# Performance work log

Measured on AMD Instinct MI355X. Metric: run time of the kernel, lower is better.

The kernel has to match this reference:

```python
import jax, jax.numpy as jnp
import numpy as np

B, D, K = 32768, 32, 32


def setup_inputs() -> dict:
    key = jax.random.key(0)
    k_x, k_w1, k_w2, k_w3, k_b = jax.random.split(key, 5)
    return {
        "X": jax.random.normal(k_x, (B, D), dtype=jnp.float32),
        "W1": jax.random.normal(k_w1, (D, K), dtype=jnp.float32) * 0.1,
        "W2": jax.random.normal(k_w2, (D, D, K), dtype=jnp.float32) * 0.05,
        "W3": jax.random.normal(k_w3, (D, D, D, K), dtype=jnp.float32) * 0.02,
        "bias": jax.random.normal(k_b, (1, K), dtype=jnp.float32) * 0.1,
    }


def reference(X, W1, W2, W3, bias):
    # order-1 term: addmm(bias, X, W1)  -> [B, K]
    out = bias + X @ W1
    # per-sample outer product X_b X_b^T, [B, D, D]. The torch code builds the
    # full cross-batch mode_dot tensor and keeps only the diagonal
    # (einsum('iik->ik')); mathematically that equals this direct contraction.
    outer = jnp.einsum("bi,bj->bij", X, X)
    out = out + jnp.einsum("bij,ijk->bk", outer, W2)
    # order-3 trilinear term: staged to avoid [B,D,D,D] intermediates.
    t3 = jnp.einsum("bij,ijkl->bkl", outer, W3)  # [B, D, K]
    out = out + jnp.einsum("bkl,bk->bl", t3, X)  # [B, K]
    return out
```

## Files before the change

### kernel.cpp

```cpp
#include <hip/hip_runtime.h>
#include <hip/hip_fp16.h>


typedef __attribute__((ext_vector_type(8))) _Float16 f16x8;
typedef __attribute__((ext_vector_type(16))) float f32x16;

#define NPAIR 561
#define NB 4
#define PAIR_BYTES 2560
#define BATCH_BYTES (NB * PAIR_BYTES)
#define NBATCH 36

union H2V { __half2 h2[4]; f16x8 v; };

__global__ void ntl_prep(const float* __restrict__ W1, const float* __restrict__ W2,
                         const float* __restrict__ W3, __half* __restrict__ Gimg) {
    int tid = blockIdx.x * 256 + threadIdx.x;
    if (tid >= NPAIR * 40 * 32) return;
    int col = tid & 31;
    int k   = (tid >> 5) % 40;
    int m   = tid / (40 * 32);
    int i = 0, rem = m;
    while (rem >= 33 - i) { rem -= 33 - i; ++i; }
    int j = i + rem;
    float v = 0.f;
    if (k < 32) {
        if (j < 32) {
            v = W3[((i * 32 + j) * 32 + k) * 32 + col];
            if (i != j) v += W3[((j * 32 + i) * 32 + k) * 32 + col];
        } else if (i < 32) {
            v = W2[(i * 32 + k) * 32 + col];
        } else {
            v = W1[k * 32 + col];
        }
    }
    Gimg[m * 1280 + col * 40 + k] = __float2half(v);
}

__global__ __launch_bounds__(512, 2) void ntl_main(const float* __restrict__ X,
                                                   const float* __restrict__ bias,
                                                   const __half* __restrict__ Gimg,
                                                   float* __restrict__ out) {
    __shared__ __half xbuf[128 * 34];
    __shared__ __align__(16) unsigned char gbuf[4][2][BATCH_BYTES];

    const int tid = (int)threadIdx.x;
    const int w   = tid >> 6;
    const int l   = tid & 63;
    const int g   = w >> 1;
    const int gw  = w & 1;
    const int h   = l >> 5;
    const int lr  = l & 31;
    const long rowbase = (long)blockIdx.x * 128;

    for (int idx = tid; idx < 128 * 32; idx += 512) {
        int r = idx >> 5, c = idx & 31;
        xbuf[r * 34 + c] = __float2half(X[(rowbase + r) * 32 + c]);
    }
    if (tid < 128) xbuf[tid * 34 + 32] = __float2half(1.0f);

    __half2 xk0[8], xk1[8];
#define LOADX(XK, TROW)                                                          \
    {                                                                            \
        const float* xp = X + (rowbase + gw * 64 + (TROW) + lr) * 32;            \
        float4 f0 = *(const float4*)(xp + 8 * h);                                \
        float4 f1 = *(const float4*)(xp + 8 * h + 4);                            \
        float4 f2 = *(const float4*)(xp + 16 + 8 * h);                           \
        float4 f3 = *(const float4*)(xp + 16 + 8 * h + 4);                       \
        XK[0] = __halves2half2(__float2half(f0.x), __float2half(f0.y));          \
        XK[1] = __halves2half2(__float2half(f0.z), __float2half(f0.w));          \
        XK[2] = __halves2half2(__float2half(f1.x), __float2half(f1.y));          \
        XK[3] = __halves2half2(__float2half(f1.z), __float2half(f1.w));          \
        XK[4] = __halves2half2(__float2half(f2.x), __float2half(f2.y));          \
        XK[5] = __halves2half2(__float2half(f2.z), __float2half(f2.w));          \
        XK[6] = __halves2half2(__float2half(f3.x), __float2half(f3.y));          \
        XK[7] = __halves2half2(__float2half(f3.z), __float2half(f3.w));          \
    }
    LOADX(xk0, 0)
    LOADX(xk1, 32)

    f32x16 acc0, acc1;
#pragma unroll
    for (int q = 0; q < 16; ++q) { acc0[q] = 0.f; acc1[q] = 0.f; }

    const int m0      = (g == 0) ? 0 : (141 + 140 * (g - 1));
    const int myPairs = (g == 0) ? 141 : 140;
    const int myNb    = (myPairs + NB - 1) / NB;

    int pi = 0, rem = m0;
    while (rem >= 33 - pi) { rem -= 33 - pi; ++pi; }
    int pj = pi + rem;

    const unsigned char* gsrc = (const unsigned char*)Gimg;
    auto stage = [&](int bb, int dbuf) {
        int cnt = myPairs - bb * NB; if (cnt > NB) cnt = NB;
        if (cnt <= 0) return;
        int bytes = cnt * PAIR_BYTES;
        const unsigned char* src = gsrc + (size_t)(m0 + bb * NB) * PAIR_BYTES;
        unsigned char* dst = &gbuf[g][dbuf][0];
        for (int ofs = gw * 1024; ofs < bytes; ofs += 2048) {
            __builtin_amdgcn_global_load_lds(
                (const __attribute__((address_space(1))) unsigned int*)(src + ofs + l * 16),
                (__attribute__((address_space(3))) unsigned int*)(dst + ofs),
                16, 0, 0);
        }
    };

    stage(0, 0);
    __syncthreads();

    for (int b = 0; b < NBATCH; ++b) {
        if (b + 1 < myNb) stage(b + 1, (b + 1) & 1);
        int cnt = myPairs - b * NB; if (cnt > NB) cnt = NB;
        const unsigned char* gb = &gbuf[g][b & 1][0];
        for (int s = 0; s < cnt; ++s) {
            const int xr0 = (gw * 64 + lr) * 34;
            const int xr1 = xr0 + 32 * 34;
            __half2 p20 = __half2half2(__hmul(xbuf[xr0 + pi], xbuf[xr0 + pj]));
            __half2 p21 = __half2half2(__hmul(xbuf[xr1 + pi], xbuf[xr1 + pj]));
            const f16x8 b0 = *(const f16x8*)(gb + s * PAIR_BYTES + lr * 80 + 16 * h);
            const f16x8 b1 = *(const f16x8*)(gb + s * PAIR_BYTES + lr * 80 + 32 + 16 * h);
            H2V a;
            a.h2[0] = __hmul2(p20, xk0[0]); a.h2[1] = __hmul2(p20, xk0[1]);
            a.h2[2] = __hmul2(p20, xk0[2]); a.h2[3] = __hmul2(p20, xk0[3]);
            acc0 = __builtin_amdgcn_mfma_f32_32x32x16_f16(a.v, b0, acc0, 0, 0, 0);
            a.h2[0] = __hmul2(p20, xk0[4]); a.h2[1] = __hmul2(p20, xk0[5]);
            a.h2[2] = __hmul2(p20, xk0[6]); a.h2[3] = __hmul2(p20, xk0[7]);
            acc0 = __builtin_amdgcn_mfma_f32_32x32x16_f16(a.v, b1, acc0, 0, 0, 0);
            a.h2[0] = __hmul2(p21, xk1[0]); a.h2[1] = __hmul2(p21, xk1[1]);
            a.h2[2] = __hmul2(p21, xk1[2]); a.h2[3] = __hmul2(p21, xk1[3]);
            acc1 = __builtin_amdgcn_mfma_f32_32x32x16_f16(a.v, b0, acc1, 0, 0, 0);
            a.h2[0] = __hmul2(p21, xk1[4]); a.h2[1] = __hmul2(p21, xk1[5]);
            a.h2[2] = __hmul2(p21, xk1[6]); a.h2[3] = __hmul2(p21, xk1[7]);
            acc1 = __builtin_amdgcn_mfma_f32_32x32x16_f16(a.v, b1, acc1, 0, 0, 0);
            ++pj; if (pj > 32) { ++pi; pj = pi; }
        }
        __syncthreads();
    }

    float* red = (float*)&gbuf[0][0][0];
    if (g >= 1) {
        int base = ((g - 1) * 2 + gw) * 2 * 16 * 64;
#pragma unroll
        for (int r = 0; r < 16; ++r) red[base + (0 * 16 + r) * 64 + l] = acc0[r];
#pragma unroll
        for (int r = 0; r < 16; ++r) red[base + (1 * 16 + r) * 64 + l] = acc1[r];
    }
    __syncthreads();
    if (g == 0) {
        float bcol = bias[lr];
#pragma unroll
        for (int r = 0; r < 16; ++r) {
            int rowoff = (r & 3) + 8 * (r >> 2) + 4 * h;
            {
                float v = acc0[r] + bcol;
#pragma unroll
                for (int sg = 0; sg < 3; ++sg)
                    v += red[((sg * 2 + gw) * 2 + 0) * 16 * 64 + r * 64 + l];
                out[(rowbase + gw * 64 + rowoff) * 32 + lr] = v;
            }
            {
                float v = acc1[r] + bcol;
#pragma unroll
                for (int sg = 0; sg < 3; ++sg)
                    v += red[((sg * 2 + gw) * 2 + 1) * 16 * 64 + r * 64 + l];
                out[(rowbase + gw * 64 + 32 + rowoff) * 32 + lr] = v;
            }
        }
    }
}

extern "C" void kernel_launch(void* const* d_in, const int* in_sizes, int n_in,
                              void* d_out, int out_size, void* d_ws, size_t ws_size,
                              hipStream_t stream) {
    const float* X    = (const float*)d_in[0];
    const float* W1   = (const float*)d_in[1];
    const float* W2   = (const float*)d_in[2];
    const float* W3   = (const float*)d_in[3];
    const float* bias = (const float*)d_in[4];
    float* out = (float*)d_out;
    __half* Gimg = (__half*)d_ws;

    int prep_threads = NPAIR * 40 * 32;
    ntl_prep<<<dim3((prep_threads + 255) / 256), dim3(256), 0, stream>>>(W1, W2, W3, Gimg);
    ntl_main<<<dim3(256), dim3(512), 0, stream>>>(X, bias, Gimg, out);
}
```

Measured before the change: 66.27 us.

## Drop LDS staging of weights, load B fragments directly and reorder pairs by runs

```diff
diff --git a/kernel.cpp b/kernel.cpp
--- a/kernel.cpp
+++ b/kernel.cpp
@@ -5,44 +5,83 @@
 typedef __attribute__((ext_vector_type(8))) _Float16 f16x8;
 typedef __attribute__((ext_vector_type(16))) float f32x16;
 
-#define NPAIR 561
-#define NB 4
-#define PAIR_BYTES 2560
-#define BATCH_BYTES (NB * PAIR_BYTES)
-#define NBATCH 36
-
-union H2V { __half2 h2[4]; f16x8 v; };
+union AV   { __half2 h2[4];  f16x8 v;    };
+union XROW { __half2 h2[16]; f16x8 v[4]; };
+
+__device__ const int RUNPI[4][9] = {
+    {0, 7, 8, 15, 16, 23, 24, 31, 32},
+    {1, 6, 9, 14, 17, 22, 25, 30, 0},
+    {2, 5, 10, 13, 18, 21, 26, 29, 0},
+    {3, 4, 11, 12, 19, 20, 27, 28, 0}};
+__device__ const int NRUN[4]  = {9, 8, 8, 8};
+__device__ const int GBASE[5] = {0, 141, 281, 421, 561};
 
 __global__ void ntl_prep(const float* __restrict__ W1, const float* __restrict__ W2,
                          const float* __restrict__ W3, __half* __restrict__ Gimg) {
     int tid = blockIdx.x * 256 + threadIdx.x;
-    if (tid >= NPAIR * 40 * 32) return;
-    int col = tid & 31;
-    int k   = (tid >> 5) % 40;
-    int m   = tid / (40 * 32);
-    int i = 0, rem = m;
-    while (rem >= 33 - i) { rem -= 33 - i; ++i; }
-    int j = i + rem;
-    float v = 0.f;
-    if (k < 32) {
-        if (j < 32) {
-            v = W3[((i * 32 + j) * 32 + k) * 32 + col];
-            if (i != j) v += W3[((j * 32 + i) * 32 + k) * 32 + col];
-        } else if (i < 32) {
-            v = W2[(i * 32 + k) * 32 + col];
-        } else {
-            v = W1[k * 32 + col];
-        }
-    }
-    Gimg[m * 1280 + col * 40 + k] = __float2half(v);
+    if (tid >= 561 * 1024) return;
+    int k    = tid & 31;
+    int col  = (tid >> 5) & 31;
+    int slot = tid >> 10;
+    int g = 0;
+    while (slot >= GBASE[g + 1]) ++g;
+    int s = slot - GBASE[g];
+    int r = 0, pi, len;
+    for (;;) { pi = RUNPI[g][r]; len = 33 - pi; if (s < len) break; s -= len; ++r; }
+    int j = pi + s;
+    float v;
+    if (j < 32) {
+        v = W3[((pi * 32 + j) * 32 + k) * 32 + col];
+        if (pi != j) v += W3[((j * 32 + pi) * 32 + k) * 32 + col];
+    } else if (pi < 32) {
+        v = W2[(pi * 32 + k) * 32 + col];
+    } else {
+        v = W1[k * 32 + col];
+    }
+    Gimg[slot * 1024 + (k >> 4) * 512 + col * 16 + (k & 15)] = __float2half(v);
 }
+
+
+#define XH(XR, J) (((J) & 1) ? __high2half((XR)[(J) >> 1]) : __low2half((XR)[(J) >> 1]))
+#define MM(ACC, A, B) (ACC) = __builtin_amdgcn_mfma_f32_32x32x16_f16((A), (B), (ACC), 0, 0, 0)
+
+#define PB(J)                                                                         \
+    {                                                                                 \
+        if ((J) < 32) {              \
+            if (((J) & 1) == 0) { boa = *(const f16x8*)gp; bob = *(const f16x8*)(gp + 1024); } \
+            else                { bea = *(const f16x8*)gp; beb = *(const f16x8*)(gp + 1024); } \
+            gp += 2048;                                                               \
+        }                                                                             \
+        const f16x8 Ba = ((J) & 1) ? boa : bea;                                       \
+        const f16x8 Bb = ((J) & 1) ? bob : beb;                                       \
+        if ((J) == 32) {                          \
+            MM(acc0, yk0[0].v, Ba); MM(acc0, yk0[1].v, Bb);                           \
+            MM(acc1, yk1[0].v, Ba); MM(acc1, yk1[1].v, Bb);                           \
+        } else {                                                                      \
+            __half2 xj0 = __half2half2(XH(xa.h2, (J)));                               \
+            __half2 xj1 = __half2half2(XH(xb.h2, (J)));                               \
+            AV a0, a1;                                                                \
+            a0.h2[0] = __hmul2(xj0, yk0[0].h2[0]); a0.h2[1] = __hmul2(xj0, yk0[0].h2[1]); \
+            a0.h2[2] = __hmul2(xj0, yk0[0].h2[2]); a0.h2[3] = __hmul2(xj0, yk0[0].h2[3]); \
+            MM(acc0, a0.v, Ba);                                                       \
+            a1.h2[0] = __hmul2(xj0, yk0[1].h2[0]); a1.h2[1] = __hmul2(xj0, yk0[1].h2[1]); \
+            a1.h2[2] = __hmul2(xj0, yk0[1].h2[2]); a1.h2[3] = __hmul2(xj0, yk0[1].h2[3]); \
+            MM(acc0, a1.v, Bb);                                                       \
+            a0.h2[0] = __hmul2(xj1, yk1[0].h2[0]); a0.h2[1] = __hmul2(xj1, yk1[0].h2[1]); \
+            a0.h2[2] = __hmul2(xj1, yk1[0].h2[2]); a0.h2[3] = __hmul2(xj1, yk1[0].h2[3]); \
+            MM(acc1, a0.v, Ba);                                                       \
+            a1.h2[0] = __hmul2(xj1, yk1[1].h2[0]); a1.h2[1] = __hmul2(xj1, yk1[1].h2[1]); \
+            a1.h2[2] = __hmul2(xj1, yk1[1].h2[2]); a1.h2[3] = __hmul2(xj1, yk1[1].h2[3]); \
+            MM(acc1, a1.v, Bb);                                                       \
+        }                                                                             \
+    }
 
 __global__ __launch_bounds__(512, 2) void ntl_main(const float* __restrict__ X,
                                                    const float* __restrict__ bias,
                                                    const __half* __restrict__ Gimg,
                                                    float* __restrict__ out) {
-    __shared__ __half xbuf[128 * 34];
-    __shared__ __align__(16) unsigned char gbuf[4][2][BATCH_BYTES];
+    __shared__ __half xbuf[128 * 40];
+    __shared__ float  red[12288];
 
     const int tid = (int)threadIdx.x;
     const int w   = tid >> 6;
@@ -53,92 +92,98 @@
     const int lr  = l & 31;
     const long rowbase = (long)blockIdx.x * 128;
 
-    for (int idx = tid; idx < 128 * 32; idx += 512) {
-        int r = idx >> 5, c = idx & 31;
-        xbuf[r * 34 + c] = __float2half(X[(rowbase + r) * 32 + c]);
-    }
-    if (tid < 128) xbuf[tid * 34 + 32] = __float2half(1.0f);
-
-    __half2 xk0[8], xk1[8];
-#define LOADX(XK, TROW)                                                          \
-    {                                                                            \
-        const float* xp = X + (rowbase + gw * 64 + (TROW) + lr) * 32;            \
-        float4 f0 = *(const float4*)(xp + 8 * h);                                \
-        float4 f1 = *(const float4*)(xp + 8 * h + 4);                            \
-        float4 f2 = *(const float4*)(xp + 16 + 8 * h);                           \
-        float4 f3 = *(const float4*)(xp + 16 + 8 * h + 4);                       \
-        XK[0] = __halves2half2(__float2half(f0.x), __float2half(f0.y));          \
-        XK[1] = __halves2half2(__float2half(f0.z), __float2half(f0.w));          \
-        XK[2] = __halves2half2(__float2half(f1.x), __float2half(f1.y));          \
-        XK[3] = __halves2half2(__float2half(f1.z), __float2half(f1.w));          \
-        XK[4] = __halves2half2(__float2half(f2.x), __float2half(f2.y));          \
-        XK[5] = __halves2half2(__float2half(f2.z), __float2half(f2.w));          \
-        XK[6] = __halves2half2(__float2half(f3.x), __float2half(f3.y));          \
-        XK[7] = __halves2half2(__float2half(f3.z), __float2half(f3.w));          \
-    }
-    LOADX(xk0, 0)
-    LOADX(xk1, 32)
+    {
+        int r0 = tid >> 2, cb = (tid & 3) * 8;
+        const float* xp = X + (rowbase + r0) * 32 + cb;
+        float4 f0 = *(const float4*)xp;
+        float4 f1 = *(const float4*)(xp + 4);
+        __half2* dst = (__half2*)&xbuf[r0 * 40 + cb];
+        dst[0] = __floats2half2_rn(f0.x, f0.y);
+        dst[1] = __floats2half2_rn(f0.z, f0.w);
+        dst[2] = __floats2half2_rn(f1.x, f1.y);
+        dst[3] = __floats2half2_rn(f1.z, f1.w);
+        if ((tid & 3) == 0) xbuf[r0 * 40 + 32] = __float2half(1.0f);
+    }
+    __syncthreads();
+
+    XROW xa, xb;
+    {
+        const f16x8* p0 = (const f16x8*)&xbuf[(gw * 64 + lr) * 40];
+        const f16x8* p1 = (const f16x8*)&xbuf[(gw * 64 + 32 + lr) * 40];
+        xa.v[0] = p0[0]; xa.v[1] = p0[1]; xa.v[2] = p0[2]; xa.v[3] = p0[3];
+        xb.v[0] = p1[0]; xb.v[1] = p1[1]; xb.v[2] = p1[2]; xb.v[3] = p1[3];
+    }
+
+    AV xk0[2], xk1[2];
+#pragma unroll
+    for (int q = 0; q < 4; ++q) {
+        xk0[0].h2[q] = h ? xa.h2[4 + q]  : xa.h2[q];
+        xk0[1].h2[q] = h ? xa.h2[12 + q] : xa.h2[8 + q];
+        xk1[0].h2[q] = h ? xb.h2[4 + q]  : xb.h2[q];
+        xk1[1].h2[q] = h ? xb.h2[12 + q] : xb.h2[8 + q];
+    }
 
     f32x16 acc0, acc1;
 #pragma unroll
     for (int q = 0; q < 16; ++q) { acc0[q] = 0.f; acc1[q] = 0.f; }
 
-    const int m0      = (g == 0) ? 0 : (141 + 140 * (g - 1));
-    const int myPairs = (g == 0) ? 141 : 140;
-    const int myNb    = (myPairs + NB - 1) / NB;
-
-    int pi = 0, rem = m0;
-    while (rem >= 33 - pi) { rem -= 33 - pi; ++pi; }
-    int pj = pi + rem;
-
-    const unsigned char* gsrc = (const unsigned char*)Gimg;
-    auto stage = [&](int bb, int dbuf) {
-        int cnt = myPairs - bb * NB; if (cnt > NB) cnt = NB;
-        if (cnt <= 0) return;
-        int bytes = cnt * PAIR_BYTES;
-        const unsigned char* src = gsrc + (size_t)(m0 + bb * NB) * PAIR_BYTES;
-        unsigned char* dst = &gbuf[g][dbuf][0];
-        for (int ofs = gw * 1024; ofs < bytes; ofs += 2048) {
-            __builtin_amdgcn_global_load_lds(
-                (const __attribute__((address_space(1))) unsigned int*)(src + ofs + l * 16),
-                (__attribute__((address_space(3))) unsigned int*)(dst + ofs),
-                16, 0, 0);
+    const char* gp = (const char*)Gimg + (size_t)GBASE[g] * 2048 + lr * 32 + h * 16;
+    f16x8 bea{}, beb{}, boa{}, bob{};
+    const int nr = NRUN[g];
+
+    for (int rr = 0; rr < nr; ++rr) {
+        const int pi = RUNPI[g][rr];
+        __half2 hp0 = __half2half2(xbuf[(gw * 64 + lr) * 40 + pi]);
+        __half2 hp1 = __half2half2(xbuf[(gw * 64 + 32 + lr) * 40 + pi]);
+        AV yk0[2], yk1[2];
+#pragma unroll
+        for (int q = 0; q < 4; ++q) {
+            yk0[0].h2[q] = __hmul2(hp0, xk0[0].h2[q]);
+            yk0[1].h2[q] = __hmul2(hp0, xk0[1].h2[q]);
+            yk1[0].h2[q] = __hmul2(hp1, xk1[0].h2[q]);
+            yk1[1].h2[q] = __hmul2(hp1, xk1[1].h2[q]);
         }
-    };
-
-    stage(0, 0);
-    __syncthreads();
-
-    for (int b = 0; b < NBATCH; ++b) {
-        if (b + 1 < myNb) stage(b + 1, (b + 1) & 1);
-        int cnt = myPairs - b * NB; if (cnt > NB) cnt = NB;
-        const unsigned char* gb = &gbuf[g][b & 1][0];
-        for (int s = 0; s < cnt; ++s) {
-            const int xr0 = (gw * 64 + lr) * 34;
-            const int xr1 = xr0 + 32 * 34;
-            __half2 p20 = __half2half2(__hmul(xbuf[xr0 + pi], xbuf[xr0 + pj]));
-            __half2 p21 = __half2half2(__hmul(xbuf[xr1 + pi], xbuf[xr1 + pj]));
-            const f16x8 b0 = *(const f16x8*)(gb + s * PAIR_BYTES + lr * 80 + 16 * h);
-            const f16x8 b1 = *(const f16x8*)(gb + s * PAIR_BYTES + lr * 80 + 32 + 16 * h);
-            H2V a;
-            a.h2[0] = __hmul2(p20, xk0[0]); a.h2[1] = __hmul2(p20, xk0[1]);
-            a.h2[2] = __hmul2(p20, xk0[2]); a.h2[3] = __hmul2(p20, xk0[3]);
-            acc0 = __builtin_amdgcn_mfma_f32_32x32x16_f16(a.v, b0, acc0, 0, 0, 0);
-            a.h2[0] = __hmul2(p20, xk0[4]); a.h2[1] = __hmul2(p20, xk0[5]);
-            a.h2[2] = __hmul2(p20, xk0[6]); a.h2[3] = __hmul2(p20, xk0[7]);
-            acc0 = __builtin_amdgcn_mfma_f32_32x32x16_f16(a.v, b1, acc0, 0, 0, 0);
-            a.h2[0] = __hmul2(p21, xk1[0]); a.h2[1] = __hmul2(p21, xk1[1]);
-            a.h2[2] = __hmul2(p21, xk1[2]); a.h2[3] = __hmul2(p21, xk1[3]);
-            acc1 = __builtin_amdgcn_mfma_f32_32x32x16_f16(a.v, b0, acc1, 0, 0, 0);
-            a.h2[0] = __hmul2(p21, xk1[4]); a.h2[1] = __hmul2(p21, xk1[5]);
-            a.h2[2] = __hmul2(p21, xk1[6]); a.h2[3] = __hmul2(p21, xk1[7]);
-            acc1 = __builtin_amdgcn_mfma_f32_32x32x16_f16(a.v, b1, acc1, 0, 0, 0);
-            ++pj; if (pj > 32) { ++pi; pj = pi; }
+        if (pi & 1) { boa = *(const f16x8*)gp; bob = *(const f16x8*)(gp + 1024); }
+        else        { bea = *(const f16x8*)gp; beb = *(const f16x8*)(gp + 1024); }
+        gp += 2048;
+
+        switch (pi) {
+            case 0:  PB(0)
+            case 1:  PB(1)
+            case 2:  PB(2)
+            case 3:  PB(3)
+            case 4:  PB(4)
+            case 5:  PB(5)
+            case 6:  PB(6)
+            case 7:  PB(7)
+            case 8:  PB(8)
+            case 9:  PB(9)
+            case 10: PB(10)
+            case 11: PB(11)
+            case 12: PB(12)
+            case 13: PB(13)
+            case 14: PB(14)
+            case 15: PB(15)
+            case 16: PB(16)
+            case 17: PB(17)
+            case 18: PB(18)
+            case 19: PB(19)
+            case 20: PB(20)
+            case 21: PB(21)
+            case 22: PB(22)
+            case 23: PB(23)
+            case 24: PB(24)
+            case 25: PB(25)
+            case 26: PB(26)
+            case 27: PB(27)
+            case 28: PB(28)
+            case 29: PB(29)
+            case 30: PB(30)
+            case 31: PB(31)
+            case 32: PB(32)
         }
-        __syncthreads();
-    }
-
-    float* red = (float*)&gbuf[0][0][0];
+    }
+
     if (g >= 1) {
         int base = ((g - 1) * 2 + gw) * 2 * 16 * 64;
 #pragma unroll
@@ -178,10 +223,10 @@
     const float* W2   = (const float*)d_in[2];
     const float* W3   = (const float*)d_in[3];
     const float* bias = (const float*)d_in[4];
-    float* out = (float*)d_out;
+    float* out  = (float*)d_out;
     __half* Gimg = (__half*)d_ws;
 
-    int prep_threads = NPAIR * 40 * 32;
+    int prep_threads = 561 * 1024;
     ntl_prep<<<dim3((prep_threads + 255) / 256), dim3(256), 0, stream>>>(W1, W2, W3, Gimg);
     ntl_main<<<dim3(256), dim3(512), 0, stream>>>(X, bias, Gimg, out);
 }
```

Result: no change. 65.76 us (-0.8%).
